# Kernel tuning notes

Hardware: AMD Instinct MI355X
Metric: run time of the kernel (lower is better)

Reference implementation:

```python
import jax, jax.numpy as jnp
import numpy as np

GRID_SIZE = 5
GRID_LO, GRID_HI = -1.0, 1.0


def setup_inputs() -> dict:
    key = jax.random.key(0)
    k1, k2 = jax.random.split(key)
    B, out_dim, in_dim, H, W = 8, 64, 64, 192, 192
    G = GRID_SIZE + 1
    x = jax.random.normal(k1, (B, in_dim, H, W), dtype=jnp.float32)
    coef = jax.random.normal(k2, (B, out_dim, in_dim, G), dtype=jnp.float32) * 0.1
    return {"x": x, "coef": coef}


def reference(x, coef):
    # x: [B, in_dim, H, W]; coef: [B, out_dim, in_dim, G] with G = grid_size + 1
    G = GRID_SIZE + 1
    grid = jnp.linspace(GRID_LO, GRID_HI, G, dtype=x.dtype)
    lo, hi = grid[0], grid[-1]
    spacing = grid[1] - grid[0]

    B, in_dim, H, W = x.shape
    out_dim = coef.shape[1]
    P = H * W

    xf = x.reshape(B, in_dim, P)
    xc = jnp.clip(xf, lo, hi)
    nx = (xc - lo) / spacing                      # normalized coordinate in [0, grid_size]
    idx = jnp.clip(jnp.floor(nx).astype(jnp.int32), 0, GRID_SIZE - 1)  # left knot
    frac = nx - idx.astype(x.dtype)               # fractional offset (grad flows via nx)
    w1 = 1.0 - frac
    w2 = frac
    idx_next = jnp.clip(idx + 1, 0, GRID_SIZE)    # right knot (max index = G-1)

    # Two-hot interpolation weights over the G grid points: [B, in, P, G]
    Wt = (w1[..., None] * jax.nn.one_hot(idx, G, dtype=x.dtype)
          + w2[..., None] * jax.nn.one_hot(idx_next, G, dtype=x.dtype))

    # result[b,o,p] = sum_i sum_g Wt[b,i,p,g] * coef[b,o,i,g]
    out = jnp.einsum('bipg,boig->bop', Wt, coef)
    return out.reshape(B, out_dim, H, W)
```

## Files before the change

### kernel.cpp

```cpp
#include <hip/hip_runtime.h>
#include <stdint.h>


typedef __fp16 half8_t __attribute__((ext_vector_type(8)));
typedef __fp16 half2_t __attribute__((ext_vector_type(2)));
typedef float f32x4 __attribute__((ext_vector_type(4)));

#define NBATCH 8
#define OD 64
#define ID 64
#define PIX 36864
#define NG 6
#define PT 192
#define KI 32
#define NCHUNK 2
#define KROW 384
#define PTILES (PIX / PT)

#define CPRE_BYTES (NBATCH * OD * KROW * 2)

__global__ __launch_bounds__(256)
void prep_coef(const float* __restrict__ coef, __fp16* __restrict__ cpre) {
  int idx = blockIdx.x * 256 + threadIdx.x;
  int b = idx / (OD * KROW);
  int rem = idx % (OD * KROW);
  int o = rem / KROW;
  int k = rem % KROW;
  int c = k / 192;
  int s = k % 192;
  int g = s >> 5;
  int iof = s & 31;
  float v = coef[((size_t)(b * OD + o) * ID + c * KI + iof) * NG + g];
  cpre[idx] = (__fp16)v;
}

__global__ __launch_bounds__(256, 4)
void kan_mfma3(const float* __restrict__ x, const __fp16* __restrict__ cpre,
               float* __restrict__ out) {
  const int t = threadIdx.x;
  const int lane = t & 63;
  const int wave = t >> 6;
  const int q8 = lane >> 4;
  const int col = lane & 15;

  const int b = blockIdx.x / PTILES;
  const int pw = (blockIdx.x % PTILES) * PT + wave * 48;

  f32x4 acc[4][3];
#pragma unroll
  for (int i = 0; i < 4; ++i)
#pragma unroll
    for (int j = 0; j < 3; ++j)
      acc[i][j] = (f32x4){0.f, 0.f, 0.f, 0.f};

  const float* xb = x + (size_t)b * ID * PIX + pw + col;
  const __fp16* cb = cpre + (size_t)b * OD * KROW + q8 * 8;

#pragma unroll
  for (int c = 0; c < NCHUNK; ++c) {
    float nxv[3][8];
#pragma unroll
    for (int pti = 0; pti < 3; ++pti)
#pragma unroll
      for (int j = 0; j < 8; ++j) {
        float xv = xb[(size_t)(c * KI + q8 * 8 + j) * PIX + pti * 16];
        xv = fminf(fmaxf(xv, -1.f), 1.f);
        nxv[pti][j] = (xv + 1.f) * 2.5f;
      }

    const __fp16* cc = cb + c * 192;
#pragma unroll
    for (int ks = 0; ks < 6; ++ks) {
      half8_t bf[4];
#pragma unroll
      for (int ot = 0; ot < 4; ++ot)
        bf[ot] = *(const half8_t*)(cc + (size_t)(ot * 16 + col) * KROW + ks * 32);

      const float gf = (float)ks;
#pragma unroll
      for (int pti = 0; pti < 3; ++pti) {
        union { half2_t h2[4]; half8_t v; } au;
#pragma unroll
        for (int jj = 0; jj < 4; ++jj) {
          float h0 = fmaxf(0.f, 1.f - fabsf(nxv[pti][2 * jj] - gf));
          float h1 = fmaxf(0.f, 1.f - fabsf(nxv[pti][2 * jj + 1] - gf));
          au.h2[jj] = __builtin_amdgcn_cvt_pkrtz(h0, h1);
        }
#pragma unroll
        for (int ot = 0; ot < 4; ++ot)
          acc[ot][pti] = __builtin_amdgcn_mfma_f32_16x16x32_f16(
              au.v, bf[ot], acc[ot][pti], 0, 0, 0);
      }
    }
  }

  float* ob = out + (size_t)b * OD * PIX + pw + q8 * 4;
#pragma unroll
  for (int ot = 0; ot < 4; ++ot)
#pragma unroll
    for (int pti = 0; pti < 3; ++pti)
      *(f32x4*)(ob + (size_t)(ot * 16 + col) * PIX + pti * 16) = acc[ot][pti];
}

#define AROW 104
#define XROW 18
__global__ __launch_bounds__(256, 2)
void kan_mfma_fb(const float* __restrict__ x, const float* __restrict__ coef,
                 float* __restrict__ out) {
  const int t = threadIdx.x;
  const int lane = t & 63;
  const int wave = t >> 6;
  const int q8 = lane >> 4;
  const int col = lane & 15;
  const int bid = blockIdx.x;
  const int b = bid / PTILES;
  const int p0 = (bid % PTILES) * PT;

  __shared__ __fp16 A_lds[OD][AROW] __attribute__((aligned(16)));
  __shared__ float nxf[PT][XROW] __attribute__((aligned(16)));

  f32x4 acc[4][3];
#pragma unroll
  for (int i = 0; i < 4; ++i)
#pragma unroll
    for (int j = 0; j < 3; ++j) acc[i][j] = (f32x4){0.f, 0.f, 0.f, 0.f};

  const float* xb = x + (size_t)b * ID * PIX + p0;
  const float* cb = coef + (size_t)b * OD * ID * NG;
  const int iof0 = (q8 & 1) * 8;
  const int ghalf = q8 >> 1;

  for (int c = 0; c < 4; ++c) {
    const int i0 = c * 16;
    __syncthreads();
#pragma unroll
    for (int j = 0; j < 12; ++j) {
      int lin = j * 256 + t;
      int p = lin % PT;
      int iof = lin / PT;
      float xvv = xb[(size_t)(i0 + iof) * PIX + p];
      xvv = fminf(fmaxf(xvv, -1.f), 1.f);
      nxf[p][iof] = (xvv + 1.f) * 2.5f;
    }
    {
      const int o = t >> 2;
      const int r0 = (t & 3) * 24;
      const float* crow = cb + o * (ID * NG) + i0 * NG + r0;
#pragma unroll
      for (int j = 0; j < 24; ++j) {
        int r = r0 + j;
        int iof = r / 6;
        int g = r - iof * 6;
        A_lds[o][g * 16 + iof] = (__fp16)crow[j];
      }
    }
    __syncthreads();

    float nxv[3][8];
#pragma unroll
    for (int pti = 0; pti < 3; ++pti) {
      int p = wave * 48 + pti * 16 + col;
#pragma unroll
      for (int j = 0; j < 8; ++j) nxv[pti][j] = nxf[p][iof0 + j];
    }
#pragma unroll
    for (int ks = 0; ks < 3; ++ks) {
      half8_t af[4];
#pragma unroll
      for (int ot = 0; ot < 4; ++ot)
        af[ot] = *(const half8_t*)&A_lds[ot * 16 + col][ks * 32 + q8 * 8];
      const float gf = (float)(2 * ks + ghalf);
#pragma unroll
      for (int pti = 0; pti < 3; ++pti) {
        union { half2_t h2[4]; half8_t v; } bu;
#pragma unroll
        for (int jj = 0; jj < 4; ++jj) {
          float h0 = fmaxf(0.f, 1.f - fabsf(nxv[pti][2 * jj] - gf));
          float h1 = fmaxf(0.f, 1.f - fabsf(nxv[pti][2 * jj + 1] - gf));
          bu.h2[jj] = __builtin_amdgcn_cvt_pkrtz(h0, h1);
        }
#pragma unroll
        for (int ot = 0; ot < 4; ++ot)
          acc[ot][pti] = __builtin_amdgcn_mfma_f32_16x16x32_f16(
              af[ot], bu.v, acc[ot][pti], 0, 0, 0);
      }
    }
  }
  float* ob = out + (size_t)b * OD * PIX + p0;
#pragma unroll
  for (int ot = 0; ot < 4; ++ot)
#pragma unroll
    for (int pti = 0; pti < 3; ++pti) {
      int p = wave * 48 + pti * 16 + col;
#pragma unroll
      for (int r = 0; r < 4; ++r)
        ob[(size_t)(ot * 16 + q8 * 4 + r) * PIX + p] = acc[ot][pti][r];
    }
}

extern "C" void kernel_launch(void* const* d_in, const int* in_sizes, int n_in,
                              void* d_out, int out_size, void* d_ws, size_t ws_size,
                              hipStream_t stream) {
  const float* x = (const float*)d_in[0];
  const float* coef = (const float*)d_in[1];
  float* out = (float*)d_out;
  if (ws_size >= (size_t)CPRE_BYTES) {
    __fp16* cpre = (__fp16*)d_ws;
    hipLaunchKernelGGL(prep_coef, dim3((NBATCH * OD * KROW) / 256), dim3(256), 0,
                       stream, coef, cpre);
    hipLaunchKernelGGL(kan_mfma3, dim3(NBATCH * PTILES), dim3(256), 0, stream, x,
                       cpre, out);
  } else {
    hipLaunchKernelGGL(kan_mfma_fb, dim3(NBATCH * PTILES), dim3(256), 0, stream,
                       x, coef, out);
  }
}
```

Measured before the change: 175.5 us.

## Load x with vector loads up front and transpose through per-wave LDS

```diff
diff --git a/kernel.cpp b/kernel.cpp
--- a/kernel.cpp
+++ b/kernel.cpp
@@ -5,6 +5,7 @@
 typedef __fp16 half8_t __attribute__((ext_vector_type(8)));
 typedef __fp16 half2_t __attribute__((ext_vector_type(2)));
 typedef float f32x4 __attribute__((ext_vector_type(4)));
+typedef float f32x2 __attribute__((ext_vector_type(2)));
 
 #define NBATCH 8
 #define OD 64
@@ -13,9 +14,9 @@
 #define NG 6
 #define PT 192
 #define KI 32
-#define NCHUNK 2
 #define KROW 384
 #define PTILES (PIX / PT)
+#define LS 50
 
 #define CPRE_BYTES (NBATCH * OD * KROW * 2)
 
@@ -34,8 +35,8 @@
   cpre[idx] = (__fp16)v;
 }
 
-__global__ __launch_bounds__(256, 4)
-void kan_mfma3(const float* __restrict__ x, const __fp16* __restrict__ cpre,
+__global__ __launch_bounds__(256, 3)
+void kan_mfma5(const float* __restrict__ x, const __fp16* __restrict__ cpre,
                float* __restrict__ out) {
   const int t = threadIdx.x;
   const int lane = t & 63;
@@ -46,6 +47,27 @@
   const int b = blockIdx.x / PTILES;
   const int pw = (blockIdx.x % PTILES) * PT + wave * 48;
 
+  __shared__ float lds_all[4][KI * LS];
+  float* __restrict__ nxs = lds_all[wave];
+
+  int li[6], lpc[6];
+#pragma unroll
+  for (int j = 0; j < 6; ++j) {
+    int u = j * 64 + lane;
+    li[j] = u / 12;
+    lpc[j] = u % 12;
+  }
+
+  const float* xb = x + (size_t)b * ID * PIX + pw;
+
+  f32x4 xr0[6], xr1[6];
+#pragma unroll
+  for (int j = 0; j < 6; ++j)
+    xr0[j] = *(const f32x4*)(xb + (size_t)li[j] * PIX + lpc[j] * 4);
+#pragma unroll
+  for (int j = 0; j < 6; ++j)
+    xr1[j] = *(const f32x4*)(xb + (size_t)(KI + li[j]) * PIX + lpc[j] * 4);
+
   f32x4 acc[4][3];
 #pragma unroll
   for (int i = 0; i < 4; ++i)
@@ -53,20 +75,30 @@
     for (int j = 0; j < 3; ++j)
       acc[i][j] = (f32x4){0.f, 0.f, 0.f, 0.f};
 
-  const float* xb = x + (size_t)b * ID * PIX + pw + col;
   const __fp16* cb = cpre + (size_t)b * OD * KROW + q8 * 8;
 
 #pragma unroll
-  for (int c = 0; c < NCHUNK; ++c) {
+  for (int c = 0; c < 2; ++c) {
+#pragma unroll
+    for (int j = 0; j < 6; ++j) {
+      f32x4 v = (c == 0) ? xr0[j] : xr1[j];
+      f32x4 n;
+#pragma unroll
+      for (int r = 0; r < 4; ++r) {
+        float xv = fminf(fmaxf(v[r], -1.f), 1.f);
+        n[r] = (xv + 1.f) * 2.5f;
+      }
+      int base = li[j] * LS + lpc[j] * 4;
+      *(f32x2*)&nxs[base] = (f32x2){n[0], n[1]};
+      *(f32x2*)&nxs[base + 2] = (f32x2){n[2], n[3]};
+    }
+
     float nxv[3][8];
 #pragma unroll
     for (int pti = 0; pti < 3; ++pti)
 #pragma unroll
-      for (int j = 0; j < 8; ++j) {
-        float xv = xb[(size_t)(c * KI + q8 * 8 + j) * PIX + pti * 16];
-        xv = fminf(fmaxf(xv, -1.f), 1.f);
-        nxv[pti][j] = (xv + 1.f) * 2.5f;
-      }
+      for (int j = 0; j < 8; ++j)
+        nxv[pti][j] = nxs[(q8 * 8 + j) * LS + pti * 16 + col];
 
     const __fp16* cc = cb + c * 192;
 #pragma unroll
@@ -208,7 +240,7 @@
     __fp16* cpre = (__fp16*)d_ws;
     hipLaunchKernelGGL(prep_coef, dim3((NBATCH * OD * KROW) / 256), dim3(256), 0,
                        stream, coef, cpre);
-    hipLaunchKernelGGL(kan_mfma3, dim3(NBATCH * PTILES), dim3(256), 0, stream, x,
+    hipLaunchKernelGGL(kan_mfma5, dim3(NBATCH * PTILES), dim3(256), 0, stream, x,
                        cpre, out);
   } else {
     hipLaunchKernelGGL(kan_mfma_fb, dim3(NBATCH * PTILES), dim3(256), 0, stream,
```

Result: faster. 164.0 us (-6.6%).
